# Kernel optimization log

Measured on AMD Instinct MI355X. Metric: run time of the kernel, lower is better.

The kernel has to match this reference:

```python
import math
import jax, jax.numpy as jnp
import numpy as np

DIM = 512
HEADS = 8
HEAD_DIM = DIM // HEADS


def get_slopes(n):
    def pow2(n):
        start = 2 ** (-2 ** (-(math.log2(n) - 3)))
        return [start * start ** i for i in range(n)]
    if math.log2(n).is_integer():
        return pow2(n)
    c = 2 ** math.floor(math.log2(n))
    return pow2(c) + get_slopes(2 * c)[0::2][: n - c]


def setup_inputs() -> dict:
    key = jax.random.key(0)
    ks = jax.random.split(key, 12)
    b, n, d = 2, 4096, DIM
    s = 1.0 / math.sqrt(d)
    inp = {
        "x": jax.random.normal(ks[0], (b, n, d), jnp.float32),
        # coords in a ~[0,100) spatial range (tile grid coordinates)
        "coords": jax.random.uniform(ks[1], (b, n, 2), jnp.float32) * 100.0,
        "Wq": jax.random.normal(ks[2], (d, d), jnp.float32) * s,
        "bq": jnp.zeros((d,), jnp.float32),
        "Wk": jax.random.normal(ks[3], (d, d), jnp.float32) * s,
        "bk": jnp.zeros((d,), jnp.float32),
        "Wv": jax.random.normal(ks[4], (d, d), jnp.float32) * s,
        "bv": jnp.zeros((d,), jnp.float32),
        "Wp": jax.random.normal(ks[5], (d, d), jnp.float32) * s,
        "bp": jnp.zeros((d,), jnp.float32),
        "slopes": jnp.asarray(get_slopes(HEADS), jnp.float32),  # [h]
    }
    return inp


def reference(x, coords, Wq, bq, Wk, bk, Wv, bv, Wp, bp, slopes):
    b, n_q, d = x.shape
    h, hd = HEADS, HEAD_DIM
    # self-attention: context = x, context_coords = coords
    q = (x @ Wq + bq).reshape(b, n_q, h, hd).transpose(0, 2, 1, 3)  # b h nq hd
    k = (x @ Wk + bk).reshape(b, n_q, h, hd).transpose(0, 2, 1, 3)
    v = (x @ Wv + bv).reshape(b, n_q, h, hd).transpose(0, 2, 1, 3)
    # Euclidean-distance ALiBi bias: [b, h, nq, nk]
    diff = coords[:, :, None, :] - coords[:, None, :, :]          # b nq nk 2
    dist = jnp.sqrt(jnp.sum(diff * diff, axis=-1))                # b nq nk
    bias = -slopes[None, :, None, None] * dist[:, None, :, :]     # b h nq nk
    scores = jnp.einsum("bhqd,bhkd->bhqk", q, k) / math.sqrt(hd) + bias
    attn = jax.nn.softmax(scores, axis=-1)
    out = jnp.einsum("bhqk,bhkd->bhqd", attn, v)
    out = out.transpose(0, 2, 1, 3).reshape(b, n_q, d)
    return out @ Wp + bp
```

## Files before the change

kernel.cpp:

```cpp
#include <hip/hip_runtime.h>
#include <stdint.h>

typedef __bf16 bf16;
typedef __attribute__((ext_vector_type(8))) __bf16 bf16x8;
typedef __attribute__((ext_vector_type(4))) __bf16 bf16x4;
typedef __attribute__((ext_vector_type(4))) float f32x4;

#define DEVFN static __device__ __forceinline__

DEVFN void gload16(const bf16* g, char* l) {
  __builtin_amdgcn_global_load_lds(
      (const __attribute__((address_space(1))) void*)g,
      (__attribute__((address_space(3))) void*)l, 16, 0, 0);
}
DEVFN void gload4(const float* g, char* l) {
  __builtin_amdgcn_global_load_lds(
      (const __attribute__((address_space(1))) void*)g,
      (__attribute__((address_space(3))) void*)l, 4, 0, 0);
}

DEVFN int swz(int row, int kb) { return row * 128 + (kb ^ ((row & 7) << 4)); }

#define PS 9437184LL

__global__ __launch_bounds__(256) void prep_kernel(
    const float* __restrict__ x, const float* __restrict__ Wq,
    const float* __restrict__ Wk, const float* __restrict__ Wv,
    const float* __restrict__ Wp, bf16* __restrict__ xb,
    bf16* __restrict__ Wt, bf16* __restrict__ Wpt) {
  const int64_t tid = blockIdx.x * 256LL + threadIdx.x;
  const int64_t stride = (int64_t)gridDim.x * 256LL;
  for (int64_t i = tid; i < (8192LL * 512) / 4; i += stride) {
    float4 v = ((const float4*)x)[i];
    bf16x4 o = {(bf16)v.x, (bf16)v.y, (bf16)v.z, (bf16)v.w};
    ((bf16x4*)xb)[i] = o;
  }
  for (int64_t i = tid; i < 1536LL * 512; i += stride) {
    int c = (int)(i >> 9), k = (int)(i & 511);
    int wsel = c >> 9, cc = c & 511;
    const float* W = wsel == 0 ? Wq : (wsel == 1 ? Wk : Wv);
    Wt[i] = (bf16)W[k * 512 + cc];
  }
  for (int64_t i = tid; i < 512LL * 512; i += stride) {
    int c = (int)(i >> 9), k = (int)(i & 511);
    Wpt[i] = (bf16)Wp[k * 512 + c];
  }
}

DEVFN void gemm_main(const bf16* __restrict__ A, const bf16* __restrict__ B,
                     int rowA0, int rowB0, char* sA, char* sB, f32x4 acc[4][4],
                     int wr, int wc, int lane, int w) {
#pragma unroll
  for (int m = 0; m < 4; m++)
#pragma unroll
    for (int n = 0; n < 4; n++) acc[m][n] = (f32x4){0.f, 0.f, 0.f, 0.f};
  const int lr = lane >> 3;
  const int kswz = 8 * ((lane & 7) ^ lr);
  for (int k0 = 0; k0 < 512; k0 += 64) {
#pragma unroll
    for (int j = 0; j < 4; j++) {
      const int c = w * 4 + j;
      gload16(A + (rowA0 + c * 8 + lr) * 512 + k0 + kswz, sA + c * 1024);
      gload16(B + (rowB0 + c * 8 + lr) * 512 + k0 + kswz, sB + c * 1024);
    }
    __syncthreads();
    bf16x8 af[4][2], bfv[4][2];
#pragma unroll
    for (int m = 0; m < 4; m++)
#pragma unroll
      for (int kk = 0; kk < 2; kk++) {
        af[m][kk] = *(const bf16x8*)(sA + swz(wr * 64 + m * 16 + (lane & 15),
                                              kk * 64 + (lane >> 4) * 16));
        bfv[m][kk] = *(const bf16x8*)(sB + swz(wc * 64 + m * 16 + (lane & 15),
                                               kk * 64 + (lane >> 4) * 16));
      }
#pragma unroll
    for (int m = 0; m < 4; m++)
#pragma unroll
      for (int n = 0; n < 4; n++)
#pragma unroll
        for (int kk = 0; kk < 2; kk++)
          acc[m][n] = __builtin_amdgcn_mfma_f32_16x16x32_bf16(
              af[m][kk], bfv[n][kk], acc[m][n], 0, 0, 0);
    __syncthreads();
  }
}

__global__ __launch_bounds__(256) void qkv_gemm(
    const bf16* __restrict__ xb, const bf16* __restrict__ Wt,
    const float* __restrict__ bq, const float* __restrict__ bk,
    const float* __restrict__ bv, bf16* __restrict__ Qb, bf16* __restrict__ Kb,
    bf16* __restrict__ Vt) {
  __shared__ __align__(128) char sA[16384];
  __shared__ __align__(128) char sB[16384];
  const int lane = threadIdx.x & 63, w = threadIdx.x >> 6;
  const int wr = w >> 1, wc = w & 1;
  const int rowA0 = blockIdx.y * 128;
  const int colB0 = blockIdx.x * 128;
  f32x4 acc[4][4];
  gemm_main(xb, Wt, rowA0, colB0, sA, sB, acc, wr, wc, lane, w);
  const int which = colB0 >> 9;
  const int cc0 = colB0 & 511;
  const float* bias = which == 0 ? bq : (which == 1 ? bk : bv);
  const float QSCALE = 0.18033688011112042f;
#pragma unroll
  for (int m = 0; m < 4; m++)
#pragma unroll
    for (int n = 0; n < 4; n++)
#pragma unroll
      for (int r = 0; r < 4; r++) {
        int row = rowA0 + wr * 64 + m * 16 + (lane >> 4) * 4 + r;
        int col = cc0 + wc * 64 + n * 16 + (lane & 15);
        float v = acc[m][n][r] + bias[col];
        if (which == 0) {
          Qb[(int64_t)row * 512 + col] = (bf16)(v * QSCALE);
        } else if (which == 1) {
          Kb[(int64_t)row * 512 + col] = (bf16)v;
        } else {
          int b = row >> 12, nn = row & 4095;
          int hh = col >> 6, e = col & 63;
          Vt[(((int64_t)(b * 8 + hh)) * 64 + e) * 4096 + nn] = (bf16)v;
        }
      }
}

__global__ __launch_bounds__(256) void out_gemm(const bf16* __restrict__ Ob,
                                                const bf16* __restrict__ Wpt,
                                                const float* __restrict__ bp,
                                                float* __restrict__ out) {
  __shared__ __align__(128) char sA[16384];
  __shared__ __align__(128) char sB[16384];
  const int lane = threadIdx.x & 63, w = threadIdx.x >> 6;
  const int wr = w >> 1, wc = w & 1;
  const int rowA0 = blockIdx.y * 128;
  const int colB0 = blockIdx.x * 128;
  f32x4 acc[4][4];
  gemm_main(Ob, Wpt, rowA0, colB0, sA, sB, acc, wr, wc, lane, w);
#pragma unroll
  for (int m = 0; m < 4; m++)
#pragma unroll
    for (int n = 0; n < 4; n++)
#pragma unroll
      for (int r = 0; r < 4; r++) {
        int row = rowA0 + wr * 64 + m * 16 + (lane >> 4) * 4 + r;
        int col = colB0 + wc * 64 + n * 16 + (lane & 15);
        out[(int64_t)row * 512 + col] = acc[m][n][r] + bp[col];
      }
}

__global__ __launch_bounds__(512) void attn_kernel(
    const bf16* __restrict__ Qb, const bf16* __restrict__ Kb,
    const bf16* __restrict__ Vt, const float* __restrict__ coords,
    const float* __restrict__ slopes, char* __restrict__ part) {
  __shared__ __align__(128) char sK[2 * 8192];
  __shared__ __align__(128) char sV[2 * 8192];
  __shared__ __align__(128) char sC[2 * 512];

  const int tid = threadIdx.x;
  const int lane = tid & 63, w = tid >> 6;
  const int c = lane & 15, g = lane >> 4;

  const int id = blockIdx.x;
  const int bh = id & 15;
  const int qt = (id >> 4) & 31;
  const int ks = id >> 9;
  const int b = bh >> 3, h = bh & 7;
  const int qw = qt * 128 + w * 16;
  const int bO = b * 4096;
  const int kvs = ks * 2048;

  const float LOG2E = 1.4426950408889634f;
  const float negsl2 = -slopes[h] * LOG2E;

  bf16x8 aq[2];
  {
    int64_t base = ((int64_t)(bO + qw + c)) * 512 + h * 64 + g * 8;
    aq[0] = *(const bf16x8*)(Qb + base);
    aq[1] = *(const bf16x8*)(Qb + base + 32);
  }
  const float* cbf = coords + (int64_t)bO * 2;
  float qcx, qcy;
  {
    float2 qc = ((const float2*)cbf)[qw + c];
    qcx = qc.x;
    qcy = qc.y;
  }

  bf16x8 ones;
#pragma unroll
  for (int jj = 0; jj < 8; jj++) ones[jj] = (bf16)1.0f;

  float m2 = -1e30f;
  f32x4 o[4], osum;
#pragma unroll
  for (int n = 0; n < 4; n++) o[n] = (f32x4){0.f, 0.f, 0.f, 0.f};
  osum = (f32x4){0.f, 0.f, 0.f, 0.f};

  const bf16* Kp = Kb + (int64_t)bO * 512 + h * 64;
  const bf16* Vp = Vt + (int64_t)(b * 8 + h) * 262144;

  const int gi = w * 64 + lane;
  const int kr = gi >> 3, kj = gi & 7;
  const int pkr = ((kr >> 4) & 1) * 32 + ((kr >> 2) & 3) * 8 +
                  ((kr >> 5) & 1) * 4 + (kr & 3);
  const bf16* kq = Kp + (int64_t)(kvs + pkr) * 512 + ((kj ^ (kr & 7)) * 8);
  const bf16* vq = Vp + kr * 4096 + kvs + ((kj ^ (kr & 7)) * 8);
  const float* cq = cbf + kvs * 2 + (w & 1) * 64 + lane;

  auto STAGE = [&](int bb) {
    gload16(kq, sK + bb * 8192 + gi * 16);
    kq += 64 * 512;
    gload16(vq, sV + bb * 8192 + gi * 16);
    vq += 64;
    if (w == 2 || w == 3) {
      gload4(cq, sC + bb * 512 + (w & 1) * 256);
      cq += 128;
    }
  };

  STAGE(0);
  __syncthreads();

  const int cm = c & 7;

#define ITER(BB, DOSTAGE)                                                     \
  {                                                                           \
    if (DOSTAGE) STAGE(BB ^ 1);                                               \
    const char* kb = sK + (BB)*8192;                                          \
    const char* vb = sV + (BB)*8192;                                          \
    const char* cb0 = sC + (BB)*512;                                          \
    bf16x8 kf[4][2];                                                          \
    _Pragma("unroll") for (int t = 0; t < 4; t++) _Pragma("unroll") for (     \
        int kk = 0; kk < 2; kk++) kf[t][kk] =                                 \
        *(const bf16x8*)(kb + (t * 16 + c) * 128 +                            \
                         (((kk * 4 + g) ^ cm) * 16));                         \
    float s[4][4];                                                            \
    __builtin_amdgcn_s_setprio(1);                                            \
    _Pragma("unroll") for (int t = 0; t < 4; t++) {                           \
      f32x4 sa = (f32x4){0.f, 0.f, 0.f, 0.f};                                 \
      sa = __builtin_amdgcn_mfma_f32_16x16x32_bf16(kf[t][0], aq[0], sa, 0, 0, \
                                                   0);                        \
      sa = __builtin_amdgcn_mfma_f32_16x16x32_bf16(kf[t][1], aq[1], sa, 0, 0, \
                                                   0);                        \
      _Pragma("unroll") for (int r = 0; r < 4; r++) s[t][r] = sa[r];          \
    }                                                                         \
    __builtin_amdgcn_s_setprio(0);                                            \
    _Pragma("unroll") for (int t = 0; t < 4; t++) {                           \
      const int cbo = (t & 1) * 256 + (t >> 1) * 32 + g * 64;                 \
      f32x4 ca = *(const f32x4*)(cb0 + cbo);                                  \
      f32x4 cb2 = *(const f32x4*)(cb0 + cbo + 16);                            \
      float dx, dy;                                                           \
      dx = qcx - ca[0]; dy = qcy - ca[1];                                     \
      s[t][0] = __builtin_fmaf(__builtin_amdgcn_sqrtf(dx * dx + dy * dy),     \
                               negsl2, s[t][0]);                              \
      dx = qcx - ca[2]; dy = qcy - ca[3];                                     \
      s[t][1] = __builtin_fmaf(__builtin_amdgcn_sqrtf(dx * dx + dy * dy),     \
                               negsl2, s[t][1]);                              \
      dx = qcx - cb2[0]; dy = qcy - cb2[1];                                   \
      s[t][2] = __builtin_fmaf(__builtin_amdgcn_sqrtf(dx * dx + dy * dy),     \
                               negsl2, s[t][2]);                              \
      dx = qcx - cb2[2]; dy = qcy - cb2[3];                                   \
      s[t][3] = __builtin_fmaf(__builtin_amdgcn_sqrtf(dx * dx + dy * dy),     \
                               negsl2, s[t][3]);                              \
    }                                                                         \
    float lm =                                                                \
        fmaxf(fmaxf(fmaxf(s[0][0], s[0][1]), fmaxf(s[0][2], s[0][3])),        \
              fmaxf(fmaxf(s[1][0], s[1][1]), fmaxf(s[1][2], s[1][3])));       \
    lm = fmaxf(lm,                                                            \
               fmaxf(fmaxf(fmaxf(s[2][0], s[2][1]), fmaxf(s[2][2], s[2][3])), \
                     fmaxf(fmaxf(s[3][0], s[3][1]),                           \
                           fmaxf(s[3][2], s[3][3]))));                        \
    if (__any(lm > m2 + 8.f)) {                                               \
      float lmf = fmaxf(lm, __shfl_xor(lm, 16));                              \
      lmf = fmaxf(lmf, __shfl_xor(lmf, 32));                                  \
      float nm = fmaxf(m2, lmf);                                              \
      float sc = __builtin_amdgcn_exp2f(m2 - nm);                             \
      m2 = nm;                                                                \
      float scr[4];                                                           \
      _Pragma("unroll") for (int r = 0; r < 4; r++) scr[r] =                  \
          __shfl(sc, (lane & 48) | (4 * g + r));                              \
      _Pragma("unroll") for (int n = 0; n < 4; n++)                           \
          _Pragma("unroll") for (int r = 0; r < 4; r++) o[n][r] *= scr[r];    \
      _Pragma("unroll") for (int r = 0; r < 4; r++) osum[r] *= scr[r];        \
    }                                                                         \
    bf16x8 pa0, pa1;                                                          \
    _Pragma("unroll") for (int r = 0; r < 4; r++) {                           \
      pa0[r] = (bf16)__builtin_amdgcn_exp2f(s[0][r] - m2);                    \
      pa0[4 + r] = (bf16)__builtin_amdgcn_exp2f(s[2][r] - m2);                \
      pa1[r] = (bf16)__builtin_amdgcn_exp2f(s[1][r] - m2);                    \
      pa1[4 + r] = (bf16)__builtin_amdgcn_exp2f(s[3][r] - m2);                \
    }                                                                         \
    __builtin_amdgcn_s_setprio(1);                                            \
    _Pragma("unroll") for (int n = 0; n < 4; n++) {                           \
      const int e = n * 16 + c;                                               \
      bf16x8 vf0 = *(const bf16x8*)(vb + e * 128 + ((g ^ (e & 7)) * 16));     \
      bf16x8 vf1 =                                                            \
          *(const bf16x8*)(vb + e * 128 + (((4 + g) ^ (e & 7)) * 16));        \
      o[n] = __builtin_amdgcn_mfma_f32_16x16x32_bf16(pa0, vf0, o[n], 0, 0,    \
                                                     0);                      \
      o[n] = __builtin_amdgcn_mfma_f32_16x16x32_bf16(pa1, vf1, o[n], 0, 0,    \
                                                     0);                      \
    }                                                                         \
    osum = __builtin_amdgcn_mfma_f32_16x16x32_bf16(pa0, ones, osum, 0, 0, 0); \
    osum = __builtin_amdgcn_mfma_f32_16x16x32_bf16(pa1, ones, osum, 0, 0, 0); \
    __builtin_amdgcn_s_setprio(0);                                            \
    __syncthreads();                                                          \
  }

  for (int u = 0; u < 16; ++u) {
    ITER(0, true);
    ITER(1, (u < 15));
  }
#undef ITER

  float m2r[4];
#pragma unroll
  for (int r = 0; r < 4; r++)
    m2r[r] = __shfl(m2, (lane & 48) | (4 * g + r));
  char* pb0 = part + ks * PS + ((int64_t)bh * 4096 + qw) * 144;
#pragma unroll
  for (int r = 0; r < 4; r++) {
    char* pb = pb0 + (g * 4 + r) * 144;
    if (c == 0) {
      *(float*)pb = m2r[r];
      *((float*)pb + 1) = osum[r];
    }
#pragma unroll
    for (int n = 0; n < 4; n++)
      *(bf16*)(pb + 16 + (n * 16 + c) * 2) = (bf16)o[n][r];
  }
}

__global__ __launch_bounds__(256) void combine_kernel(
    const char* __restrict__ part, bf16* __restrict__ Ob) {
  const int t = blockIdx.x * 256 + threadIdx.x;
  const int row = t >> 3;
  const int eb = (t & 7) * 8;
  const char* p0 = part + (int64_t)row * 144;
  const char* p1 = p0 + PS;
  const float m0 = *(const float*)p0, s0 = *((const float*)p0 + 1);
  const float m1 = *(const float*)p1, s1 = *((const float*)p1 + 1);
  bf16x8 o0 = *(const bf16x8*)(p0 + 16 + eb * 2);
  bf16x8 o1 = *(const bf16x8*)(p1 + 16 + eb * 2);
  const float m = fmaxf(m0, m1);
  const float w0 = __builtin_amdgcn_exp2f(m0 - m);
  const float w1 = __builtin_amdgcn_exp2f(m1 - m);
  const float inv = 1.f / (s0 * w0 + s1 * w1);
  bf16x8 res;
#pragma unroll
  for (int j = 0; j < 8; j++)
    res[j] = (bf16)(((float)o0[j] * w0 + (float)o1[j] * w1) * inv);
  const int bh = row >> 12, q = row & 4095;
  *(bf16x8*)(Ob + ((int64_t)((bh >> 3) * 4096 + q)) * 512 + (bh & 7) * 64 +
             eb) = res;
}

extern "C" void kernel_launch(void* const* d_in, const int* in_sizes, int n_in,
                              void* d_out, int out_size, void* d_ws,
                              size_t ws_size, hipStream_t stream) {
  const float* x = (const float*)d_in[0];
  const float* coords = (const float*)d_in[1];
  const float* Wq = (const float*)d_in[2];
  const float* bq = (const float*)d_in[3];
  const float* Wk = (const float*)d_in[4];
  const float* bk = (const float*)d_in[5];
  const float* Wv = (const float*)d_in[6];
  const float* bv = (const float*)d_in[7];
  const float* Wp = (const float*)d_in[8];
  const float* bp = (const float*)d_in[9];
  const float* slopes = (const float*)d_in[10];

  char* ws = (char*)d_ws;
  bf16* xb = (bf16*)(ws);
  bf16* Wt = (bf16*)(ws + 8388608);
  bf16* Wpt = (bf16*)(ws + 9961472);
  bf16* Qb = (bf16*)(ws + 10485760);
  bf16* Kb = (bf16*)(ws + 18874368);
  bf16* Vt = (bf16*)(ws + 27262976);
  bf16* Ob = (bf16*)(ws + 35651584);
  char* part = ws + 44040192;

  hipLaunchKernelGGL(prep_kernel, dim3(1024), dim3(256), 0, stream, x, Wq, Wk,
                     Wv, Wp, xb, Wt, Wpt);
  hipLaunchKernelGGL(qkv_gemm, dim3(12, 64), dim3(256), 0, stream, xb, Wt, bq,
                     bk, bv, Qb, Kb, Vt);
  hipLaunchKernelGGL(attn_kernel, dim3(1024), dim3(512), 0, stream, Qb, Kb,
                     Vt, coords, slopes, part);
  hipLaunchKernelGGL(combine_kernel, dim3(2048), dim3(256), 0, stream, part,
                     Ob);
  hipLaunchKernelGGL(out_gemm, dim3(4, 64), dim3(256), 0, stream, Ob, Wpt, bp,
                     (float*)d_out);
}
```

Baseline: 199.9 us.

## Deepen attention K/V/coords prefetch to a four-stage ring with one barrier

Replaces the double-buffered K/V/coord staging in the attention kernel with a four-slot LDS ring and a prefetch distance of two tiles. Explicit vmcnt waits plus a single s_barrier at the top of each iteration replace the trailing __syncthreads, so loads have more time in flight before they are consumed. Coordinate staging moves from two waves issuing 4-byte LDS loads to one wave issuing 16-byte loads. The cost is more LDS per block (about 68KB), which may reduce how many blocks fit on a CU, and the hand-written waitcnt accounting is fragile.

```diff
diff --git a/kernel.cpp b/kernel.cpp
--- a/kernel.cpp
+++ b/kernel.cpp
@@ -13,10 +13,10 @@
       (const __attribute__((address_space(1))) void*)g,
       (__attribute__((address_space(3))) void*)l, 16, 0, 0);
 }
-DEVFN void gload4(const float* g, char* l) {
+DEVFN void gload16f(const float* g, char* l) {
   __builtin_amdgcn_global_load_lds(
       (const __attribute__((address_space(1))) void*)g,
-      (__attribute__((address_space(3))) void*)l, 4, 0, 0);
+      (__attribute__((address_space(3))) void*)l, 16, 0, 0);
 }
 
 DEVFN int swz(int row, int kb) { return row * 128 + (kb ^ ((row & 7) << 4)); }
@@ -152,9 +152,9 @@
     const bf16* __restrict__ Qb, const bf16* __restrict__ Kb,
     const bf16* __restrict__ Vt, const float* __restrict__ coords,
     const float* __restrict__ slopes, char* __restrict__ part) {
-  __shared__ __align__(128) char sK[2 * 8192];
-  __shared__ __align__(128) char sV[2 * 8192];
-  __shared__ __align__(128) char sC[2 * 512];
+  __shared__ __align__(128) char sK[4 * 8192];
+  __shared__ __align__(128) char sV[4 * 8192];
+  __shared__ __align__(128) char sC[4 * 1024];
 
   const int tid = threadIdx.x;
   const int lane = tid & 63, w = tid >> 6;
@@ -205,30 +205,39 @@
                   ((kr >> 5) & 1) * 4 + (kr & 3);
   const bf16* kq = Kp + (int64_t)(kvs + pkr) * 512 + ((kj ^ (kr & 7)) * 8);
   const bf16* vq = Vp + kr * 4096 + kvs + ((kj ^ (kr & 7)) * 8);
-  const float* cq = cbf + kvs * 2 + (w & 1) * 64 + lane;
+  const float* cq = cbf + kvs * 2 + (lane < 32 ? lane * 4 : 0);
 
   auto STAGE = [&](int bb) {
     gload16(kq, sK + bb * 8192 + gi * 16);
     kq += 64 * 512;
     gload16(vq, sV + bb * 8192 + gi * 16);
     vq += 64;
-    if (w == 2 || w == 3) {
-      gload4(cq, sC + bb * 512 + (w & 1) * 256);
+    if (w == 7) {
+      gload16f(cq, sC + bb * 1024);
       cq += 128;
     }
   };
 
   STAGE(0);
-  __syncthreads();
+  STAGE(1);
 
   const int cm = c & 7;
 
-#define ITER(BB, DOSTAGE)                                                     \
+#define ITER(BB, DOSTAGE, LAST)                                               \
   {                                                                           \
-    if (DOSTAGE) STAGE(BB ^ 1);                                               \
+    if (LAST) {                                                               \
+      asm volatile("s_waitcnt vmcnt(0)" ::: "memory");                        \
+    } else if (w == 7) {                                                      \
+      asm volatile("s_waitcnt vmcnt(3)" ::: "memory");                        \
+    } else {                                                                  \
+      asm volatile("s_waitcnt vmcnt(2)" ::: "memory");                        \
+    }                                                                         \
+    __builtin_amdgcn_s_barrier();                                             \
+    __builtin_amdgcn_sched_barrier(0);                                        \
+    if (DOSTAGE) STAGE(((BB) + 2) & 3);                                       \
     const char* kb = sK + (BB)*8192;                                          \
     const char* vb = sV + (BB)*8192;                                          \
-    const char* cb0 = sC + (BB)*512;                                          \
+    const char* cb0 = sC + (BB)*1024;                                         \
     bf16x8 kf[4][2];                                                          \
     _Pragma("unroll") for (int t = 0; t < 4; t++) _Pragma("unroll") for (     \
         int kk = 0; kk < 2; kk++) kf[t][kk] =                                 \
@@ -304,12 +313,14 @@
     osum = __builtin_amdgcn_mfma_f32_16x16x32_bf16(pa0, ones, osum, 0, 0, 0); \
     osum = __builtin_amdgcn_mfma_f32_16x16x32_bf16(pa1, ones, osum, 0, 0, 0); \
     __builtin_amdgcn_s_setprio(0);                                            \
-    __syncthreads();                                                          \
-  }
-
-  for (int u = 0; u < 16; ++u) {
-    ITER(0, true);
-    ITER(1, (u < 15));
+  }
+
+  for (int u = 0; u < 8; ++u) {
+    const int t0 = u * 4;
+    ITER(0, (t0 + 2 < 32), false);
+    ITER(1, (t0 + 3 < 32), false);
+    ITER(2, (t0 + 4 < 32), false);
+    ITER(3, (t0 + 5 < 32), (t0 + 3 == 31));
   }
 #undef ITER
 
```

Result: no change. 201.2 us (+0.6%).
